# Kernel tuning notes

Measured on AMD Instinct MI355X. Metric: run time of the kernel, lower is better.

Reference implementation:

```python
import jax, jax.numpy as jnp
import numpy as np

N, T, V, C_IN, C_OUT = 4, 32, 1024, 256, 64

def setup_inputs() -> dict:
    key = jax.random.key(0)
    k = jax.random.split(key, 5)
    std = np.sqrt(2.0 / (C_OUT * C_IN))  # kaiming_init: n = out*in
    return {
        "z": jax.random.normal(k[0], (N, T, V, C_IN), dtype=jnp.float32),
        "theta_w": jax.random.normal(k[1], (C_OUT, C_IN), dtype=jnp.float32) * std,
        "theta_b": jnp.zeros((C_OUT,), dtype=jnp.float32),
        "phi_w": jax.random.normal(k[2], (C_OUT, C_IN), dtype=jnp.float32) * std,
        "phi_b": jnp.zeros((C_OUT,), dtype=jnp.float32),
    }

def reference(z, theta_w, theta_b, phi_w, phi_b):
    # Linear projections: [n,t,v,c_in] -> [n,t,v,c_out]
    theta = jnp.einsum('ntvc,oc->ntvo', z, theta_w) + theta_b
    phi = jnp.einsum('ntvc,oc->ntvo', z, phi_w) + phi_b
    # Affinity: S[n,t,v,w] = theta[n,t,v,:] . phi[n,t,w,:]
    S = jnp.einsum('ntvo,ntwo->ntvw', theta, phi)
    # Row-wise softmax over last dim -> learned adjacency G
    G = jax.nn.softmax(S, axis=-1)
    return G
```

## Files before the change

### kernel.cpp

```cpp
#include <hip/hip_runtime.h>


#define LOG2E 1.44269504088896340736f

typedef float  floatx4 __attribute__((ext_vector_type(4)));
typedef short  shortx8 __attribute__((ext_vector_type(8)));

__device__ __forceinline__ unsigned short f2bf(float f) {
  unsigned int u = __builtin_bit_cast(unsigned int, f);
  u += 0x7fffu + ((u >> 16) & 1u);
  return (unsigned short)(u >> 16);
}

__device__ __forceinline__ shortx8 load_cvt_bf16x8(const float* p) {
  float4 f0 = *(const float4*)p;
  float4 f1 = *(const float4*)(p + 4);
  shortx8 a;
  a[0] = (short)f2bf(f0.x); a[1] = (short)f2bf(f0.y);
  a[2] = (short)f2bf(f0.z); a[3] = (short)f2bf(f0.w);
  a[4] = (short)f2bf(f1.x); a[5] = (short)f2bf(f1.y);
  a[6] = (short)f2bf(f1.z); a[7] = (short)f2bf(f1.w);
  return a;
}

__global__ __launch_bounds__(256, 2)
void k_proj(const float* __restrict__ z,
            const float* __restrict__ tw, const float* __restrict__ tb,
            const float* __restrict__ pw, const float* __restrict__ pb,
            unsigned short* __restrict__ theta, unsigned short* __restrict__ phi)
{
  __shared__ unsigned short Wl[128 * 256];
  const int tid  = threadIdx.x;
  const int lane = tid & 63;
  const int wv   = tid >> 6;
  const int c16  = lane & 15;
  const int q4   = lane >> 4;
  const size_t r0 = (size_t)blockIdx.x * 128;

  #pragma unroll
  for (int i = 0; i < 16; ++i) {
    int p = tid + i * 256;
    int n = p >> 5;
    int g = p & 31;
    const float* src = (n < 64) ? (tw + (size_t)n * 256 + g * 8)
                                : (pw + (size_t)(n - 64) * 256 + g * 8);
    float sc = (n < 64) ? LOG2E : 1.0f;
    float4 f0 = *(const float4*)src;
    float4 f1 = *(const float4*)(src + 4);
    union { unsigned short h[8]; int4 v; } u;
    u.h[0] = f2bf(f0.x * sc); u.h[1] = f2bf(f0.y * sc);
    u.h[2] = f2bf(f0.z * sc); u.h[3] = f2bf(f0.w * sc);
    u.h[4] = f2bf(f1.x * sc); u.h[5] = f2bf(f1.y * sc);
    u.h[6] = f2bf(f1.z * sc); u.h[7] = f2bf(f1.w * sc);
    *(int4*)(&Wl[n * 256 + ((g ^ (n & 31)) * 8)]) = u.v;
  }
  __syncthreads();

  floatx4 acc[2][8];
  #pragma unroll
  for (int rt = 0; rt < 2; ++rt)
    #pragma unroll
    for (int ct = 0; ct < 8; ++ct) acc[rt][ct] = 0.0f;

  const float* z0 = z + (r0 + (size_t)wv * 32 + c16) * 256 + q4 * 8;
  #pragma unroll
  for (int s = 0; s < 8; ++s) {
    shortx8 a0 = load_cvt_bf16x8(z0 + s * 32);
    shortx8 a1 = load_cvt_bf16x8(z0 + 16 * 256 + s * 32);
    #pragma unroll
    for (int ct = 0; ct < 8; ++ct) {
      int n = ct * 16 + c16;
      int g = s * 4 + q4;
      shortx8 b = *(const shortx8*)(&Wl[n * 256 + ((g ^ (n & 31)) * 8)]);
      acc[0][ct] = __builtin_amdgcn_mfma_f32_16x16x32_bf16(a0, b, acc[0][ct], 0, 0, 0);
      acc[1][ct] = __builtin_amdgcn_mfma_f32_16x16x32_bf16(a1, b, acc[1][ct], 0, 0, 0);
    }
  }

  #pragma unroll
  for (int ct = 0; ct < 8; ++ct) {
    int c = ct * 16 + c16;
    float bias = (c < 64) ? tb[c] * LOG2E : pb[c - 64];
    #pragma unroll
    for (int rt = 0; rt < 2; ++rt)
      #pragma unroll
      for (int r = 0; r < 4; ++r) {
        size_t gr = r0 + (size_t)wv * 32 + rt * 16 + q4 * 4 + r;
        unsigned short hv = f2bf(acc[rt][ct][r] + bias);
        if (c < 64) theta[gr * 64 + c] = hv;
        else        phi[gr * 64 + (c - 64)] = hv;
      }
  }
}

__global__ __launch_bounds__(256, 2)
void k_adj(const unsigned short* __restrict__ theta,
           const unsigned short* __restrict__ phi,
           float* __restrict__ out)
{
  __shared__ __align__(16) float redm[32][4];
  __shared__ __align__(16) float reds[32][4];
  const int tid  = threadIdx.x;
  const int lane = tid & 63;
  const int wv   = tid >> 6;
  const int c16  = lane & 15;
  const int q4   = lane >> 4;
  const int nt   = blockIdx.x >> 5;
  const int vb   = blockIdx.x & 31;

  const unsigned short* tbase =
      theta + ((size_t)nt * 1024 + vb * 32 + c16) * 64 + q4 * 8;
  const unsigned short* pbase =
      phi + ((size_t)nt * 1024 + wv * 256 + c16) * 64 + q4 * 8;

  floatx4 acc[2][16];
  #pragma unroll
  for (int rt = 0; rt < 2; ++rt)
    #pragma unroll
    for (int ct = 0; ct < 16; ++ct) acc[rt][ct] = 0.0f;

  #pragma unroll
  for (int s = 0; s < 2; ++s) {
    shortx8 a0 = *(const shortx8*)(tbase + s * 32);
    shortx8 a1 = *(const shortx8*)(tbase + 16 * 64 + s * 32);
    #pragma unroll
    for (int ct = 0; ct < 16; ++ct) {
      shortx8 b = *(const shortx8*)(pbase + (size_t)ct * 16 * 64 + s * 32);
      acc[0][ct] = __builtin_amdgcn_mfma_f32_16x16x32_bf16(a0, b, acc[0][ct], 0, 0, 0);
      acc[1][ct] = __builtin_amdgcn_mfma_f32_16x16x32_bf16(a1, b, acc[1][ct], 0, 0, 0);
    }
  }

  float rmax[2][4];
  #pragma unroll
  for (int rt = 0; rt < 2; ++rt)
    #pragma unroll
    for (int r = 0; r < 4; ++r) {
      float m = acc[rt][0][r];
      #pragma unroll
      for (int ct = 1; ct < 16; ++ct) m = fmaxf(m, acc[rt][ct][r]);
      rmax[rt][r] = m;
    }
  #pragma unroll
  for (int mask = 1; mask <= 8; mask <<= 1)
    #pragma unroll
    for (int rt = 0; rt < 2; ++rt)
      #pragma unroll
      for (int r = 0; r < 4; ++r)
        rmax[rt][r] = fmaxf(rmax[rt][r], __shfl_xor(rmax[rt][r], mask, 64));

  if (c16 == 0) {
    #pragma unroll
    for (int rt = 0; rt < 2; ++rt)
      #pragma unroll
      for (int r = 0; r < 4; ++r)
        redm[rt * 16 + q4 * 4 + r][wv] = rmax[rt][r];
  }
  __syncthreads();

  float gmax[2][4], rsum[2][4];
  #pragma unroll
  for (int rt = 0; rt < 2; ++rt)
    #pragma unroll
    for (int r = 0; r < 4; ++r) {
      float4 v = *(const float4*)(&redm[rt * 16 + q4 * 4 + r][0]);
      gmax[rt][r] = fmaxf(fmaxf(v.x, v.y), fmaxf(v.z, v.w));
      rsum[rt][r] = 0.0f;
    }

  #pragma unroll
  for (int rt = 0; rt < 2; ++rt)
    #pragma unroll
    for (int ct = 0; ct < 16; ++ct)
      #pragma unroll
      for (int r = 0; r < 4; ++r) {
        float e = exp2f(acc[rt][ct][r] - gmax[rt][r]);
        acc[rt][ct][r] = e;
        rsum[rt][r] += e;
      }
  #pragma unroll
  for (int mask = 1; mask <= 8; mask <<= 1)
    #pragma unroll
    for (int rt = 0; rt < 2; ++rt)
      #pragma unroll
      for (int r = 0; r < 4; ++r)
        rsum[rt][r] += __shfl_xor(rsum[rt][r], mask, 64);

  if (c16 == 0) {
    #pragma unroll
    for (int rt = 0; rt < 2; ++rt)
      #pragma unroll
      for (int r = 0; r < 4; ++r)
        reds[rt * 16 + q4 * 4 + r][wv] = rsum[rt][r];
  }
  __syncthreads();

  float rinv[2][4];
  #pragma unroll
  for (int rt = 0; rt < 2; ++rt)
    #pragma unroll
    for (int r = 0; r < 4; ++r) {
      float4 v = *(const float4*)(&reds[rt * 16 + q4 * 4 + r][0]);
      rinv[rt][r] = __builtin_amdgcn_rcpf(v.x + v.y + v.z + v.w);
    }

  float* ob = out + (size_t)nt * 1024 * 1024 + (size_t)vb * 32 * 1024
                  + wv * 256 + c16;
  #pragma unroll
  for (int rt = 0; rt < 2; ++rt)
    #pragma unroll
    for (int r = 0; r < 4; ++r) {
      float* orow = ob + (size_t)(rt * 16 + q4 * 4 + r) * 1024;
      float sc = rinv[rt][r];
      #pragma unroll
      for (int ct = 0; ct < 16; ++ct)
        orow[ct * 16] = acc[rt][ct][r] * sc;
    }
}

extern "C" void kernel_launch(void* const* d_in, const int* in_sizes, int n_in,
                              void* d_out, int out_size, void* d_ws, size_t ws_size,
                              hipStream_t stream) {
  const float* z  = (const float*)d_in[0];
  const float* tw = (const float*)d_in[1];
  const float* tb = (const float*)d_in[2];
  const float* pw = (const float*)d_in[3];
  const float* pb = (const float*)d_in[4];
  float* out = (float*)d_out;

  unsigned short* theta = (unsigned short*)d_ws;
  unsigned short* phi   = theta + (size_t)131072 * 64;

  k_proj<<<dim3(1024), dim3(256), 0, stream>>>(z, tw, tb, pw, pb, theta, phi);
  k_adj<<<dim3(4096), dim3(256), 0, stream>>>(theta, phi, out);
}
```

Baseline: 751.0 us.

## Swap MFMA operand order for vectorized row-major stores and halve adjacency tile

Both kernels swap the MFMA A/B operands so each lane holds four consecutive output columns of one row. This lets the projection write bf16x4 packed stores and the softmax kernel write float4 non-temporal stores instead of scattered scalar stores. The adjacency kernel now handles 16 rows per block instead of 32, with twice as many blocks and launch bounds raised to 3 blocks per CU. The row reductions also shrink from four shuffle steps to two. Fewer rows per block means phi is reloaded more often across blocks.

```diff
diff --git a/kernel.cpp b/kernel.cpp
--- a/kernel.cpp
+++ b/kernel.cpp
@@ -72,150 +72,103 @@
       int n = ct * 16 + c16;
       int g = s * 4 + q4;
       shortx8 b = *(const shortx8*)(&Wl[n * 256 + ((g ^ (n & 31)) * 8)]);
-      acc[0][ct] = __builtin_amdgcn_mfma_f32_16x16x32_bf16(a0, b, acc[0][ct], 0, 0, 0);
-      acc[1][ct] = __builtin_amdgcn_mfma_f32_16x16x32_bf16(a1, b, acc[1][ct], 0, 0, 0);
+      acc[0][ct] = __builtin_amdgcn_mfma_f32_16x16x32_bf16(b, a0, acc[0][ct], 0, 0, 0);
+      acc[1][ct] = __builtin_amdgcn_mfma_f32_16x16x32_bf16(b, a1, acc[1][ct], 0, 0, 0);
     }
   }
 
   #pragma unroll
   for (int ct = 0; ct < 8; ++ct) {
-    int c = ct * 16 + c16;
-    float bias = (c < 64) ? tb[c] * LOG2E : pb[c - 64];
+    int c0 = ct * 16 + q4 * 4;
+    const bool is_t = (c0 < 64);
+    const float* bp = is_t ? (tb + c0) : (pb + (c0 - 64));
+    float4 bias = *(const float4*)bp;
+    float sc = is_t ? LOG2E : 1.0f;
     #pragma unroll
-    for (int rt = 0; rt < 2; ++rt)
-      #pragma unroll
-      for (int r = 0; r < 4; ++r) {
-        size_t gr = r0 + (size_t)wv * 32 + rt * 16 + q4 * 4 + r;
-        unsigned short hv = f2bf(acc[rt][ct][r] + bias);
-        if (c < 64) theta[gr * 64 + c] = hv;
-        else        phi[gr * 64 + (c - 64)] = hv;
-      }
+    for (int rt = 0; rt < 2; ++rt) {
+      size_t gr = r0 + (size_t)wv * 32 + rt * 16 + c16;
+      union { unsigned short h[4]; uint2 v; } u;
+      u.h[0] = f2bf(acc[rt][ct][0] + bias.x * sc);
+      u.h[1] = f2bf(acc[rt][ct][1] + bias.y * sc);
+      u.h[2] = f2bf(acc[rt][ct][2] + bias.z * sc);
+      u.h[3] = f2bf(acc[rt][ct][3] + bias.w * sc);
+      unsigned short* dst = is_t ? theta : phi;
+      *(uint2*)(dst + gr * 64 + (c0 & 63)) = u.v;
+    }
   }
 }
 
-__global__ __launch_bounds__(256, 2)
+__global__ __launch_bounds__(256, 3)
 void k_adj(const unsigned short* __restrict__ theta,
            const unsigned short* __restrict__ phi,
            float* __restrict__ out)
 {
-  __shared__ __align__(16) float redm[32][4];
-  __shared__ __align__(16) float reds[32][4];
+  __shared__ __align__(16) float redm[16][4];
+  __shared__ __align__(16) float reds[16][4];
   const int tid  = threadIdx.x;
   const int lane = tid & 63;
   const int wv   = tid >> 6;
   const int c16  = lane & 15;
   const int q4   = lane >> 4;
-  const int nt   = blockIdx.x >> 5;
-  const int vb   = blockIdx.x & 31;
+  const int nt   = blockIdx.x >> 6;
+  const int vb   = blockIdx.x & 63;
 
   const unsigned short* tbase =
-      theta + ((size_t)nt * 1024 + vb * 32 + c16) * 64 + q4 * 8;
+      theta + ((size_t)nt * 1024 + vb * 16 + c16) * 64 + q4 * 8;
   const unsigned short* pbase =
       phi + ((size_t)nt * 1024 + wv * 256 + c16) * 64 + q4 * 8;
 
-  floatx4 acc[2][16];
+  floatx4 acc[16];
   #pragma unroll
-  for (int rt = 0; rt < 2; ++rt)
-    #pragma unroll
-    for (int ct = 0; ct < 16; ++ct) acc[rt][ct] = 0.0f;
+  for (int ct = 0; ct < 16; ++ct) acc[ct] = 0.0f;
 
   #pragma unroll
   for (int s = 0; s < 2; ++s) {
-    shortx8 a0 = *(const shortx8*)(tbase + s * 32);
-    shortx8 a1 = *(const shortx8*)(tbase + 16 * 64 + s * 32);
+    shortx8 t = *(const shortx8*)(tbase + s * 32);
     #pragma unroll
     for (int ct = 0; ct < 16; ++ct) {
-      shortx8 b = *(const shortx8*)(pbase + (size_t)ct * 16 * 64 + s * 32);
-      acc[0][ct] = __builtin_amdgcn_mfma_f32_16x16x32_bf16(a0, b, acc[0][ct], 0, 0, 0);
-      acc[1][ct] = __builtin_amdgcn_mfma_f32_16x16x32_bf16(a1, b, acc[1][ct], 0, 0, 0);
+      shortx8 p = *(const shortx8*)(pbase + (size_t)ct * 16 * 64 + s * 32);
+      acc[ct] = __builtin_amdgcn_mfma_f32_16x16x32_bf16(p, t, acc[ct], 0, 0, 0);
     }
   }
 
-  float rmax[2][4];
+  float m = acc[0][0];
   #pragma unroll
-  for (int rt = 0; rt < 2; ++rt)
+  for (int ct = 0; ct < 16; ++ct)
+    #pragma unroll
+    for (int r = 0; r < 4; ++r) m = fmaxf(m, acc[ct][r]);
+  m = fmaxf(m, __shfl_xor(m, 16, 64));
+  m = fmaxf(m, __shfl_xor(m, 32, 64));
+  if (lane < 16) redm[c16][wv] = m;
+  __syncthreads();
+
+  float4 mv = *(const float4*)(&redm[c16][0]);
+  float gmax = fmaxf(fmaxf(mv.x, mv.y), fmaxf(mv.z, mv.w));
+
+  float sum = 0.0f;
+  #pragma unroll
+  for (int ct = 0; ct < 16; ++ct)
     #pragma unroll
     for (int r = 0; r < 4; ++r) {
-      float m = acc[rt][0][r];
-      #pragma unroll
-      for (int ct = 1; ct < 16; ++ct) m = fmaxf(m, acc[rt][ct][r]);
-      rmax[rt][r] = m;
+      float e = exp2f(acc[ct][r] - gmax);
+      acc[ct][r] = e;
+      sum += e;
     }
-  #pragma unroll
-  for (int mask = 1; mask <= 8; mask <<= 1)
-    #pragma unroll
-    for (int rt = 0; rt < 2; ++rt)
-      #pragma unroll
-      for (int r = 0; r < 4; ++r)
-        rmax[rt][r] = fmaxf(rmax[rt][r], __shfl_xor(rmax[rt][r], mask, 64));
-
-  if (c16 == 0) {
-    #pragma unroll
-    for (int rt = 0; rt < 2; ++rt)
-      #pragma unroll
-      for (int r = 0; r < 4; ++r)
-        redm[rt * 16 + q4 * 4 + r][wv] = rmax[rt][r];
-  }
+  sum += __shfl_xor(sum, 16, 64);
+  sum += __shfl_xor(sum, 32, 64);
+  if (lane < 16) reds[c16][wv] = sum;
   __syncthreads();
 
-  float gmax[2][4], rsum[2][4];
+  float4 sv = *(const float4*)(&reds[c16][0]);
+  float rinv = __builtin_amdgcn_rcpf(sv.x + sv.y + sv.z + sv.w);
+
+  float* ob = out + (size_t)nt * 1024 * 1024
+                  + (size_t)(vb * 16 + c16) * 1024 + wv * 256 + q4 * 4;
   #pragma unroll
-  for (int rt = 0; rt < 2; ++rt)
-    #pragma unroll
-    for (int r = 0; r < 4; ++r) {
-      float4 v = *(const float4*)(&redm[rt * 16 + q4 * 4 + r][0]);
-      gmax[rt][r] = fmaxf(fmaxf(v.x, v.y), fmaxf(v.z, v.w));
-      rsum[rt][r] = 0.0f;
-    }
-
-  #pragma unroll
-  for (int rt = 0; rt < 2; ++rt)
-    #pragma unroll
-    for (int ct = 0; ct < 16; ++ct)
-      #pragma unroll
-      for (int r = 0; r < 4; ++r) {
-        float e = exp2f(acc[rt][ct][r] - gmax[rt][r]);
-        acc[rt][ct][r] = e;
-        rsum[rt][r] += e;
-      }
-  #pragma unroll
-  for (int mask = 1; mask <= 8; mask <<= 1)
-    #pragma unroll
-    for (int rt = 0; rt < 2; ++rt)
-      #pragma unroll
-      for (int r = 0; r < 4; ++r)
-        rsum[rt][r] += __shfl_xor(rsum[rt][r], mask, 64);
-
-  if (c16 == 0) {
-    #pragma unroll
-    for (int rt = 0; rt < 2; ++rt)
-      #pragma unroll
-      for (int r = 0; r < 4; ++r)
-        reds[rt * 16 + q4 * 4 + r][wv] = rsum[rt][r];
+  for (int ct = 0; ct < 16; ++ct) {
+    floatx4 g = acc[ct] * rinv;
+    __builtin_nontemporal_store(g, (floatx4*)(ob + ct * 16));
   }
-  __syncthreads();
-
-  float rinv[2][4];
-  #pragma unroll
-  for (int rt = 0; rt < 2; ++rt)
-    #pragma unroll
-    for (int r = 0; r < 4; ++r) {
-      float4 v = *(const float4*)(&reds[rt * 16 + q4 * 4 + r][0]);
-      rinv[rt][r] = __builtin_amdgcn_rcpf(v.x + v.y + v.z + v.w);
-    }
-
-  float* ob = out + (size_t)nt * 1024 * 1024 + (size_t)vb * 32 * 1024
-                  + wv * 256 + c16;
-  #pragma unroll
-  for (int rt = 0; rt < 2; ++rt)
-    #pragma unroll
-    for (int r = 0; r < 4; ++r) {
-      float* orow = ob + (size_t)(rt * 16 + q4 * 4 + r) * 1024;
-      float sc = rinv[rt][r];
-      #pragma unroll
-      for (int ct = 0; ct < 16; ++ct)
-        orow[ct * 16] = acc[rt][ct][r] * sc;
-    }
 }
 
 extern "C" void kernel_launch(void* const* d_in, const int* in_sizes, int n_in,
@@ -232,5 +185,5 @@
   unsigned short* phi   = theta + (size_t)131072 * 64;
 
   k_proj<<<dim3(1024), dim3(256), 0, stream>>>(z, tw, tb, pw, pb, theta, phi);
-  k_adj<<<dim3(4096), dim3(256), 0, stream>>>(theta, phi, out);
+  k_adj<<<dim3(8192), dim3(256), 0, stream>>>(theta, phi, out);
 }
```

New measurement: 748.2 us. About the same (-0.4%).
